# Performance work log

Measured on AMD Instinct MI355X. Metric: run time of the kernel, lower is better.

## Reference

```python
import jax, jax.numpy as jnp
import numpy as np

B, D, L, NH = 8, 1024, 1024, 8
DK = D // NH  # = Dv = 128
NEG = -1e30


def setup_inputs() -> dict:
    key = jax.random.key(0)
    kx, km, kq, kk, kv, ko = jax.random.split(key, 6)
    x = jax.random.normal(kx, (B, D, L), dtype=jnp.float32)
    # binary mask over sequence positions (float, as in the torch code)
    mask = (jax.random.uniform(km, (B, L)) > 0.1).astype(jnp.float32)
    # xavier-ish scale for per-head projections, kaiming-ish for Wo
    s_qkv = np.sqrt(2.0 / (D + DK)).astype(np.float32)
    Wq = jax.random.normal(kq, (NH, D, DK), dtype=jnp.float32) * s_qkv
    Wk = jax.random.normal(kk, (NH, D, DK), dtype=jnp.float32) * s_qkv
    Wv = jax.random.normal(kv, (NH, D, DK), dtype=jnp.float32) * s_qkv
    Wo = jax.random.normal(ko, (D, DK * NH), dtype=jnp.float32) * np.sqrt(2.0 / D).astype(np.float32)
    return {"x": x, "mask": mask, "Wq": Wq, "Wk": Wk, "Wv": Wv, "Wo": Wo}


def reference(x, mask, Wq, Wk, Wv, Wo):
    # x: [B, D, L] -> [B, L, D]
    xt = jnp.swapaxes(x, 1, 2)
    scale = 1.0 / np.sqrt(DK).astype(np.float32)
    # batched per-head projections (equivalent to the per-head loop)
    q = jnp.einsum("bld,hdk->bhlk", xt, Wq)  # [B,H,L,Dk]
    k = jnp.einsum("bld,hdk->bhlk", xt, Wk)
    v = jnp.einsum("bld,hdk->bhlk", xt, Wv)
    # scores[b,h,q_pos,k_pos]
    scores = jnp.einsum("bhqd,bhkd->bhqk", q, k) * scale
    # mask.unsqueeze(2) in torch -> additive mask along the QUERY axis
    scores = scores + (1.0 - mask)[:, None, :, None] * NEG
    # faithful quirk: softmax over dim=1 of [B,Lq,Lk] == query axis (axis=2 here)
    attn = jax.nn.softmax(scores, axis=2)
    heads = jnp.einsum("bhqk,bhkd->bhqd", attn, v)  # [B,H,L,Dv]
    head = jnp.swapaxes(heads, 1, 2).reshape(B, L, NH * DK)  # concat heads
    out = head @ Wo  # [B, L, D]
    return jnp.swapaxes(out, 1, 2)  # [B, D, L]
```

## Files before the change

kernel.cpp:

```cpp
#include <hip/hip_runtime.h>

typedef short bf16x8 __attribute__((ext_vector_type(8)));
typedef float f32x4 __attribute__((ext_vector_type(4)));

#define MASK_NEG (-1e30f)

__device__ __forceinline__ unsigned short f2bf(float f) {
  union { float f; unsigned u; } v; v.f = f;
  unsigned r = v.u + 0x7fffu + ((v.u >> 16) & 1u);
  return (unsigned short)(r >> 16);
}

__device__ __forceinline__ float bf2f(unsigned short u) {
  union { unsigned u; float f; } v; v.u = ((unsigned)u) << 16;
  return v.f;
}

__device__ __forceinline__ void gl_lds16(const void* g, void* l) {
  __builtin_amdgcn_global_load_lds(
      (__attribute__((address_space(1))) void*)(void*)g,
      (__attribute__((address_space(3))) void*)l, 16, 0, 0);
}

__device__ __forceinline__ void transpose_tile(
    const float* __restrict__ s, unsigned short* __restrict__ d,
    int R, int C, int x0, int y0, int t, float tile[64][65]) {
  {
    const int r = t >> 4, c4 = (t & 15) * 4;
    for (int it = 0; it < 4; ++it) {
      const int rr = r + it * 16;
      const float4 v = *(const float4*)(s + (size_t)(y0 + rr) * C + x0 + c4);
      tile[rr][c4 + 0] = v.x; tile[rr][c4 + 1] = v.y;
      tile[rr][c4 + 2] = v.z; tile[rr][c4 + 3] = v.w;
    }
  }
  __syncthreads();
  {
    const int cc = t >> 4, r4 = (t & 15) * 4;
    for (int it = 0; it < 4; ++it) {
      const int c = cc + it * 16;
      ushort4 o;
      o.x = f2bf(tile[r4 + 0][c]); o.y = f2bf(tile[r4 + 1][c]);
      o.z = f2bf(tile[r4 + 2][c]); o.w = f2bf(tile[r4 + 3][c]);
      *(ushort4*)(d + (size_t)(x0 + c) * R + y0 + r4) = o;
    }
  }
}

__global__ __launch_bounds__(256) void transpose_x_wo(
    const float* __restrict__ x, const float* __restrict__ Wo,
    unsigned short* __restrict__ xt, unsigned short* __restrict__ Wot) {
  __shared__ float tile[64][65];
  const int z = blockIdx.z;
  const float* s = (z < 8) ? (x + (size_t)z * 1048576) : Wo;
  unsigned short* d = (z < 8) ? (xt + (size_t)z * 1048576) : Wot;
  transpose_tile(s, d, 1024, 1024, blockIdx.x * 64, blockIdx.y * 64,
                 threadIdx.x, tile);
}

__global__ __launch_bounds__(256) void transpose_w24(
    const float* __restrict__ Wq, const float* __restrict__ Wk,
    const float* __restrict__ Wv, unsigned short* __restrict__ WqkvT) {
  __shared__ float tile[64][65];
  const int z = blockIdx.z;
  const int sel = z >> 3, h = z & 7;
  const float* base = (sel == 0) ? Wq : (sel == 1) ? Wk : Wv;
  const float* s = base + (size_t)h * 131072;
  unsigned short* d = WqkvT + (size_t)z * 131072;
  transpose_tile(s, d, 1024, 128, blockIdx.x * 64, blockIdx.y * 64,
                 threadIdx.x, tile);
}

template<bool F32OUT>
__global__ __launch_bounds__(256) void gemm_tn(
    const unsigned short* __restrict__ A, const unsigned short* __restrict__ B,
    void* __restrict__ Cv,
    int K, int ldA, int ldB, int ldC, float scale,
    long sAl, long sAb, long sAh,
    long sBl, long sBb, long sBh,
    long sCl, long sCb, long sCh,
    int zbase, int zdiv)
{
  __shared__ unsigned short As[128 * 64];
  __shared__ unsigned short Bs[128 * 64];
  const int z = blockIdx.z;
  const int g = zbase + z;
  const int gb = g / zdiv, gh = g % zdiv;
  const unsigned short* Ab = A + (size_t)z * sAl + (size_t)gb * sAb + (size_t)gh * sAh;
  const unsigned short* Bb = B + (size_t)z * sBl + (size_t)gb * sBb + (size_t)gh * sBh;
  const int m0 = blockIdx.y * 128, n0 = blockIdx.x * 128;
  const int t = threadIdx.x;
  const int lane = t & 63;
  const int wave = t >> 6;
  const int wm = wave >> 1, wn = wave & 1;

  const int sr2 = t >> 3;
  const int ss8 = t & 7;
  const int sq8 = ss8 ^ (sr2 & 7);

  const unsigned short* ap0 = Ab + (size_t)(m0 +  0 + sr2) * ldA + sq8 * 8;
  const unsigned short* ap1 = Ab + (size_t)(m0 + 32 + sr2) * ldA + sq8 * 8;
  const unsigned short* ap2 = Ab + (size_t)(m0 + 64 + sr2) * ldA + sq8 * 8;
  const unsigned short* ap3 = Ab + (size_t)(m0 + 96 + sr2) * ldA + sq8 * 8;
  const unsigned short* bp0 = Bb + (size_t)(n0 +  0 + sr2) * ldB + sq8 * 8;
  const unsigned short* bp1 = Bb + (size_t)(n0 + 32 + sr2) * ldB + sq8 * 8;
  const unsigned short* bp2 = Bb + (size_t)(n0 + 64 + sr2) * ldB + sq8 * 8;
  const unsigned short* bp3 = Bb + (size_t)(n0 + 96 + sr2) * ldB + sq8 * 8;

  char* asd0 = (char*)As +     0 + t * 16;
  char* asd1 = (char*)As +  4096 + t * 16;
  char* asd2 = (char*)As +  8192 + t * 16;
  char* asd3 = (char*)As + 12288 + t * 16;
  char* bsd0 = (char*)Bs +     0 + t * 16;
  char* bsd1 = (char*)Bs +  4096 + t * 16;
  char* bsd2 = (char*)Bs +  8192 + t * 16;
  char* bsd3 = (char*)Bs + 12288 + t * 16;

  const int tq = lane & 15, qd = lane >> 4;

  f32x4 acc[4][4];
  #pragma unroll
  for (int i = 0; i < 4; ++i)
    #pragma unroll
    for (int j = 0; j < 4; ++j)
      acc[i][j] = f32x4{0.f, 0.f, 0.f, 0.f};

  const int kIters = K >> 6;
  for (int kt = 0; kt < kIters; ++kt) {
    __syncthreads();
    gl_lds16(ap0, asd0); gl_lds16(ap1, asd1);
    gl_lds16(ap2, asd2); gl_lds16(ap3, asd3);
    gl_lds16(bp0, bsd0); gl_lds16(bp1, bsd1);
    gl_lds16(bp2, bsd2); gl_lds16(bp3, bsd3);
    ap0 += 64; ap1 += 64; ap2 += 64; ap3 += 64;
    bp0 += 64; bp1 += 64; bp2 += 64; bp3 += 64;
    __builtin_amdgcn_s_waitcnt(0x0f70);
    __syncthreads();

    #pragma unroll
    for (int kk = 0; kk < 2; ++kk) {
      bf16x8 af[4], bfr[4];
      #pragma unroll
      for (int i = 0; i < 4; ++i) {
        const int R = wm * 64 + i * 16 + tq;
        const int slot = (kk * 4 + qd) ^ (R & 7);
        af[i] = *(const bf16x8*)(As + R * 64 + slot * 8);
      }
      #pragma unroll
      for (int j = 0; j < 4; ++j) {
        const int R = wn * 64 + j * 16 + tq;
        const int slot = (kk * 4 + qd) ^ (R & 7);
        bfr[j] = *(const bf16x8*)(Bs + R * 64 + slot * 8);
      }
      #pragma unroll
      for (int i = 0; i < 4; ++i)
        #pragma unroll
        for (int j = 0; j < 4; ++j)
          acc[i][j] = __builtin_amdgcn_mfma_f32_16x16x32_bf16(af[i], bfr[j], acc[i][j], 0, 0, 0);
    }
  }

  const size_t cOff = (size_t)z * sCl + (size_t)gb * sCb + (size_t)gh * sCh;
  #pragma unroll
  for (int i = 0; i < 4; ++i) {
    const int row = m0 + wm * 64 + i * 16 + qd * 4;
    #pragma unroll
    for (int j = 0; j < 4; ++j) {
      const int col = n0 + wn * 64 + j * 16 + tq;
      if constexpr (F32OUT) {
        float* C = (float*)Cv + cOff;
        #pragma unroll
        for (int rr = 0; rr < 4; ++rr)
          C[(size_t)(row + rr) * ldC + col] = acc[i][j][rr] * scale;
      } else {
        unsigned short* C = (unsigned short*)Cv + cOff;
        #pragma unroll
        for (int rr = 0; rr < 4; ++rr)
          C[(size_t)(row + rr) * ldC + col] = f2bf(acc[i][j][rr] * scale);
      }
    }
  }
}

__global__ __launch_bounds__(256) void gemm_scores_fused(
    const unsigned short* __restrict__ QKV,
    unsigned short* __restrict__ E, float* __restrict__ colsum,
    const float* __restrict__ mask, int zbase)
{
  __shared__ unsigned short As[4096];
  __shared__ unsigned short Bs[4096];
  const int z = blockIdx.z;
  const int g = zbase + z;
  const int b = g >> 3, h = g & 7;
  const unsigned short* Ab = QKV + (size_t)b * 3145728 + (size_t)h * 131072;
  const unsigned short* Bb = Ab + 1048576;
  const int m0 = blockIdx.y * 128, n0 = blockIdx.x * 128;
  const int t = threadIdx.x;
  const int lane = t & 63;
  const int wave = t >> 6;
  const int wm = wave >> 1, wn = wave & 1;

  const int sr = t >> 2, ss = t & 3;
  const int sq = ss ^ (sr & 3) ^ ((sr >> 2) & 3);

  const unsigned short* ap0 = Ab + (size_t)(m0 + sr) * 128 + sq * 8;
  const unsigned short* ap1 = Ab + (size_t)(m0 + sr + 64) * 128 + sq * 8;
  const unsigned short* bp0 = Bb + (size_t)(n0 + sr) * 128 + sq * 8;
  const unsigned short* bp1 = Bb + (size_t)(n0 + sr + 64) * 128 + sq * 8;

  char* asd0 = (char*)As + t * 16;
  char* asd1 = (char*)As + 4096 + t * 16;
  char* bsd0 = (char*)Bs + t * 16;
  char* bsd1 = (char*)Bs + 4096 + t * 16;

  const int tq = lane & 15, qd = lane >> 4;
  const int slot = qd ^ (tq & 3) ^ ((tq >> 2) & 3);

  f32x4 acc[4][4];
  #pragma unroll
  for (int i = 0; i < 4; ++i)
    #pragma unroll
    for (int j = 0; j < 4; ++j)
      acc[i][j] = f32x4{0.f, 0.f, 0.f, 0.f};

  #pragma unroll
  for (int kt = 0; kt < 4; ++kt) {
    __syncthreads();
    gl_lds16(ap0, asd0); gl_lds16(ap1, asd1);
    gl_lds16(bp0, bsd0); gl_lds16(bp1, bsd1);
    ap0 += 32; ap1 += 32; bp0 += 32; bp1 += 32;
    __builtin_amdgcn_s_waitcnt(0x0f70);
    __syncthreads();

    bf16x8 af[4], bfr[4];
    #pragma unroll
    for (int i = 0; i < 4; ++i)
      af[i] = *(const bf16x8*)(As + ((wm * 64 + i * 16 + tq) * 32 + slot * 8));
    #pragma unroll
    for (int j = 0; j < 4; ++j)
      bfr[j] = *(const bf16x8*)(Bs + ((wn * 64 + j * 16 + tq) * 32 + slot * 8));
    #pragma unroll
    for (int i = 0; i < 4; ++i)
      #pragma unroll
      for (int j = 0; j < 4; ++j)
        acc[i][j] = __builtin_amdgcn_mfma_f32_16x16x32_bf16(af[i], bfr[j], acc[i][j], 0, 0, 0);
  }

  unsigned short* Ep = E + (size_t)z * 1048576;
  float* cs = colsum + (size_t)g * 1024;
  const float scl = 0.08838834764831845f;
  const float* mrow = mask + (size_t)b * 1024;

  float cp[4] = {0.f, 0.f, 0.f, 0.f};
  #pragma unroll
  for (int i = 0; i < 4; ++i) {
    const int row0 = m0 + wm * 64 + i * 16 + qd * 4;
    const float4 m4 = *(const float4*)(mrow + row0);
    const float aq[4] = {(1.f - m4.x) * MASK_NEG - 20.f, (1.f - m4.y) * MASK_NEG - 20.f,
                         (1.f - m4.z) * MASK_NEG - 20.f, (1.f - m4.w) * MASK_NEG - 20.f};
    #pragma unroll
    for (int rr = 0; rr < 4; ++rr) {
      unsigned short* erow = Ep + (size_t)(row0 + rr) * 1024 + n0 + wn * 64 + tq;
      #pragma unroll
      for (int j = 0; j < 4; ++j) {
        const float e = __expf(acc[i][j][rr] * scl + aq[rr]);
        cp[j] += e;
        erow[j * 16] = f2bf(e);
      }
    }
  }
  #pragma unroll
  for (int j = 0; j < 4; ++j) {
    float v = cp[j];
    v += __shfl_xor(v, 16, 64);
    v += __shfl_xor(v, 32, 64);
    if (qd == 0)
      atomicAdd(&cs[n0 + wn * 64 + j * 16 + tq], v);
  }
}

__global__ __launch_bounds__(256) void tvscale(
    const unsigned short* __restrict__ QKV, unsigned short* __restrict__ Vp,
    const float* __restrict__ colsum, int zbase)
{
  __shared__ unsigned short tile[64][72];
  const int z = blockIdx.z;
  const int g = zbase + z;
  const int b = g >> 3, h = g & 7;
  const unsigned short* S = QKV + (size_t)b * 3145728 + (size_t)(16 + h) * 131072;
  unsigned short* D = Vp + (size_t)g * 131072;
  const float* cs = colsum + (size_t)g * 1024;
  const int l0 = blockIdx.x * 64;
  const int d0 = blockIdx.y * 64;
  const int t = threadIdx.x;
  {
    const int r = t >> 4, c4 = (t & 15) * 4;
    for (int it = 0; it < 4; ++it) {
      const int rr = r + it * 16;
      const ushort4 v = *(const ushort4*)(S + (size_t)(l0 + rr) * 128 + d0 + c4);
      *(ushort4*)&tile[rr][c4] = v;
    }
  }
  __syncthreads();
  {
    const int cc = t >> 4, r4 = (t & 15) * 4;
    const float4 c4v = *(const float4*)(cs + l0 + r4);
    for (int it = 0; it < 4; ++it) {
      const int c = cc + it * 16;
      ushort4 o;
      o.x = f2bf(bf2f(tile[r4 + 0][c]) / c4v.x);
      o.y = f2bf(bf2f(tile[r4 + 1][c]) / c4v.y);
      o.z = f2bf(bf2f(tile[r4 + 2][c]) / c4v.z);
      o.w = f2bf(bf2f(tile[r4 + 3][c]) / c4v.w);
      *(ushort4*)(D + (size_t)(d0 + c) * 1024 + l0 + r4) = o;
    }
  }
}

extern "C" void kernel_launch(void* const* d_in, const int* in_sizes, int n_in,
                              void* d_out, int out_size, void* d_ws, size_t ws_size,
                              hipStream_t stream) {
  const float* x    = (const float*)d_in[0];
  const float* mask = (const float*)d_in[1];
  const float* Wq   = (const float*)d_in[2];
  const float* Wk   = (const float*)d_in[3];
  const float* Wv   = (const float*)d_in[4];
  const float* Wo   = (const float*)d_in[5];
  float* out = (float*)d_out;

  char* p = (char*)d_ws;
  unsigned short* xt    = (unsigned short*)p; p += 16777216;
  unsigned short* WqkvT = (unsigned short*)p; p += 6291456;
  unsigned short* Wot   = (unsigned short*)p; p += 2097152;
  unsigned short* QKV   = (unsigned short*)p; p += 50331648;
  unsigned short* Vp    = (unsigned short*)p; p += 16777216;
  unsigned short* Hp    = (unsigned short*)p; p += 16777216;
  float* colsum = (float*)p; p += 262144;
  const size_t fixedBytes = (size_t)(p - (char*)d_ws);

  long nbh = 1;
  if (ws_size > fixedBytes) {
    nbh = (long)((ws_size - fixedBytes) / 2097152);
    if (nbh < 1) nbh = 1;
    if (nbh > 64) nbh = 64;
  }
  unsigned short* Ep = (unsigned short*)p;

  hipMemsetAsync(colsum, 0, 262144, stream);

  transpose_x_wo<<<dim3(16, 16, 9), 256, 0, stream>>>(x, Wo, xt, Wot);
  transpose_w24<<<dim3(2, 16, 24), 256, 0, stream>>>(Wq, Wk, Wv, WqkvT);

  gemm_tn<false><<<dim3(1, 8, 192), 256, 0, stream>>>(
      xt, WqkvT, (void*)QKV, 1024, 1024, 1024, 128, 1.f,
      0L, 1048576L, 0L,  0L, 0L, 131072L,  0L, 3145728L, 131072L, 0, 24);

  for (int s0 = 0; s0 < 64; s0 += (int)nbh) {
    const int cnt = (int)(((64 - s0) < nbh) ? (64 - s0) : nbh);
    gemm_scores_fused<<<dim3(8, 8, cnt), 256, 0, stream>>>(QKV, Ep, colsum, mask, s0);
    tvscale<<<dim3(16, 2, cnt), 256, 0, stream>>>(QKV, Vp, colsum, s0);
    gemm_tn<false><<<dim3(1, 8, cnt), 256, 0, stream>>>(
        Ep, Vp, (void*)Hp, 1024, 1024, 1024, 1024, 1.f,
        1048576L, 0L, 0L,  0L, 1048576L, 131072L,  0L, 1048576L, 128L, s0, 8);
  }
  gemm_tn<true><<<dim3(8, 8, 8), 256, 0, stream>>>(
      Wot, Hp, (void*)out, 1024, 1024, 1024, 1024, 1.f,
      0L, 0L, 0L,  0L, 1048576L, 0L,  0L, 1048576L, 0L, 0, 1);
}
```

Measured before the change: 298.9 us.

## Load full K=128 tiles once and stage score output through LDS for vector stores

The scores kernel now loads the whole 128x128 Q and K tiles into 64KB of LDS in one pass with an XOR swizzle, which removes the per-k-step barrier and reload loop. The exp'd bf16 scores are then written to a padded LDS tile and copied out with 16-byte row-contiguous global stores, replacing the scattered 2-byte stores. In exchange, LDS use per block grows from 16KB to 64KB, which reduces occupancy, and all load latency is exposed up front with no overlap.

```diff
diff --git a/kernel.cpp b/kernel.cpp
--- a/kernel.cpp
+++ b/kernel.cpp
@@ -2,6 +2,7 @@
 
 typedef short bf16x8 __attribute__((ext_vector_type(8)));
 typedef float f32x4 __attribute__((ext_vector_type(4)));
+typedef unsigned short u16x8 __attribute__((ext_vector_type(8)));
 
 #define MASK_NEG (-1e30f)
 
@@ -187,8 +188,9 @@
     unsigned short* __restrict__ E, float* __restrict__ colsum,
     const float* __restrict__ mask, int zbase)
 {
-  __shared__ unsigned short As[4096];
-  __shared__ unsigned short Bs[4096];
+  __shared__ unsigned short sbuf[32768];
+  unsigned short* As = sbuf;
+  unsigned short* Bs = sbuf + 16384;
   const int z = blockIdx.z;
   const int g = zbase + z;
   const int b = g >> 3, h = g & 7;
@@ -199,22 +201,20 @@
   const int lane = t & 63;
   const int wave = t >> 6;
   const int wm = wave >> 1, wn = wave & 1;
-
-  const int sr = t >> 2, ss = t & 3;
-  const int sq = ss ^ (sr & 3) ^ ((sr >> 2) & 3);
-
-  const unsigned short* ap0 = Ab + (size_t)(m0 + sr) * 128 + sq * 8;
-  const unsigned short* ap1 = Ab + (size_t)(m0 + sr + 64) * 128 + sq * 8;
-  const unsigned short* bp0 = Bb + (size_t)(n0 + sr) * 128 + sq * 8;
-  const unsigned short* bp1 = Bb + (size_t)(n0 + sr + 64) * 128 + sq * 8;
-
-  char* asd0 = (char*)As + t * 16;
-  char* asd1 = (char*)As + 4096 + t * 16;
-  char* bsd0 = (char*)Bs + t * 16;
-  char* bsd1 = (char*)Bs + 4096 + t * 16;
-
   const int tq = lane & 15, qd = lane >> 4;
-  const int slot = qd ^ (tq & 3) ^ ((tq >> 2) & 3);
+
+  const unsigned short* Aq = Ab + (size_t)m0 * 128;
+  const unsigned short* Bk = Bb + (size_t)n0 * 128;
+  #pragma unroll
+  for (int it = 0; it < 8; ++it) {
+    const int c = it * 256 + t;
+    const int row = c >> 4;
+    const int src = (c ^ (c >> 4)) & 15;
+    gl_lds16(Aq + (size_t)row * 128 + src * 8, (char*)As + c * 16);
+    gl_lds16(Bk + (size_t)row * 128 + src * 8, (char*)Bs + c * 16);
+  }
+  __builtin_amdgcn_s_waitcnt(0x0f70);
+  __syncthreads();
 
   f32x4 acc[4][4];
   #pragma unroll
@@ -224,21 +224,20 @@
       acc[i][j] = f32x4{0.f, 0.f, 0.f, 0.f};
 
   #pragma unroll
-  for (int kt = 0; kt < 4; ++kt) {
-    __syncthreads();
-    gl_lds16(ap0, asd0); gl_lds16(ap1, asd1);
-    gl_lds16(bp0, bsd0); gl_lds16(bp1, bsd1);
-    ap0 += 32; ap1 += 32; bp0 += 32; bp1 += 32;
-    __builtin_amdgcn_s_waitcnt(0x0f70);
-    __syncthreads();
-
+  for (int kk = 0; kk < 4; ++kk) {
     bf16x8 af[4], bfr[4];
     #pragma unroll
-    for (int i = 0; i < 4; ++i)
-      af[i] = *(const bf16x8*)(As + ((wm * 64 + i * 16 + tq) * 32 + slot * 8));
-    #pragma unroll
-    for (int j = 0; j < 4; ++j)
-      bfr[j] = *(const bf16x8*)(Bs + ((wn * 64 + j * 16 + tq) * 32 + slot * 8));
+    for (int i = 0; i < 4; ++i) {
+      const int R = wm * 64 + i * 16 + tq;
+      const int slot = (kk * 4 + qd) ^ (R & 15);
+      af[i] = *(const bf16x8*)(As + R * 128 + slot * 8);
+    }
+    #pragma unroll
+    for (int j = 0; j < 4; ++j) {
+      const int R = wn * 64 + j * 16 + tq;
+      const int slot = (kk * 4 + qd) ^ (R & 15);
+      bfr[j] = *(const bf16x8*)(Bs + R * 128 + slot * 8);
+    }
     #pragma unroll
     for (int i = 0; i < 4; ++i)
       #pragma unroll
@@ -246,7 +245,9 @@
         acc[i][j] = __builtin_amdgcn_mfma_f32_16x16x32_bf16(af[i], bfr[j], acc[i][j], 0, 0, 0);
   }
 
-  unsigned short* Ep = E + (size_t)z * 1048576;
+  __syncthreads();
+
+  unsigned short* T = sbuf;
   float* cs = colsum + (size_t)g * 1024;
   const float scl = 0.08838834764831845f;
   const float* mrow = mask + (size_t)b * 1024;
@@ -254,18 +255,18 @@
   float cp[4] = {0.f, 0.f, 0.f, 0.f};
   #pragma unroll
   for (int i = 0; i < 4; ++i) {
-    const int row0 = m0 + wm * 64 + i * 16 + qd * 4;
-    const float4 m4 = *(const float4*)(mrow + row0);
+    const int r0 = wm * 64 + i * 16 + qd * 4;
+    const float4 m4 = *(const float4*)(mrow + m0 + r0);
     const float aq[4] = {(1.f - m4.x) * MASK_NEG - 20.f, (1.f - m4.y) * MASK_NEG - 20.f,
                          (1.f - m4.z) * MASK_NEG - 20.f, (1.f - m4.w) * MASK_NEG - 20.f};
     #pragma unroll
     for (int rr = 0; rr < 4; ++rr) {
-      unsigned short* erow = Ep + (size_t)(row0 + rr) * 1024 + n0 + wn * 64 + tq;
       #pragma unroll
       for (int j = 0; j < 4; ++j) {
+        const int cl = wn * 64 + j * 16 + tq;
         const float e = __expf(acc[i][j][rr] * scl + aq[rr]);
         cp[j] += e;
-        erow[j * 16] = f2bf(e);
+        T[(r0 + rr) * 136 + cl] = f2bf(e);
       }
     }
   }
@@ -276,6 +277,16 @@
     v += __shfl_xor(v, 32, 64);
     if (qd == 0)
       atomicAdd(&cs[n0 + wn * 64 + j * 16 + tq], v);
+  }
+  __syncthreads();
+
+  unsigned short* Ep = E + (size_t)z * 1048576 + (size_t)m0 * 1024 + n0;
+  #pragma unroll
+  for (int r = 0; r < 8; ++r) {
+    const int c = r * 256 + t;
+    const int row = c >> 4, sl = c & 15;
+    u16x8 v = *(const u16x8*)(T + row * 136 + sl * 8);
+    *(u16x8*)(Ep + (size_t)row * 1024 + sl * 8) = v;
   }
 }
 
```

Result: no change. 297.3 us (-0.5%).
